# Performance work log

Hardware: AMD Instinct MI355X
Metric: run time of the kernel (lower is better)

## Reference

```python
import jax, jax.numpy as jnp
import numpy as np

N = 100000
E = 1600000
IN_C = 128
HID = 256
OUT_C = 128
MLP_H = 512  # hidden_state_factor * hidden_channels


def _mk_mlp(key, d_in, d_h, d_out):
    ks = jax.random.split(key, 3)
    s = 0.02
    return (
        jax.random.normal(ks[0], (d_in, d_h), jnp.float32) * s, jnp.zeros((d_h,), jnp.float32),
        jax.random.normal(ks[1], (d_h, d_h), jnp.float32) * s, jnp.zeros((d_h,), jnp.float32),
        jax.random.normal(ks[2], (d_h, d_out), jnp.float32) * s, jnp.zeros((d_out,), jnp.float32),
    )


def _mlp(x, w1, b1, w2, b2, w3, b3, last_act):
    h = jax.nn.relu(x @ w1 + b1)
    h = jax.nn.relu(h @ w2 + b2)
    h = h @ w3 + b3
    return jax.nn.relu(h) if last_act else h


def setup_inputs() -> dict:
    key = jax.random.key(0)
    kx, ke, k1, k2, k3 = jax.random.split(key, 5)
    x = jax.random.normal(kx, (N, IN_C), jnp.float32)
    edge_index = jax.random.randint(ke, (2, E), 0, N, jnp.int64)
    enc = _mk_mlp(k1, IN_C, MLP_H, HID)
    conv = _mk_mlp(k2, HID, MLP_H, HID)
    dec = _mk_mlp(k3, HID, MLP_H, OUT_C)
    names_enc = ["enc_w1", "enc_b1", "enc_w2", "enc_b2", "enc_w3", "enc_b3"]
    names_conv = ["conv_w1", "conv_b1", "conv_w2", "conv_b2", "conv_w3", "conv_b3"]
    names_dec = ["dec_w1", "dec_b1", "dec_w2", "dec_b2", "dec_w3", "dec_b3"]
    d = {"x": x, "edge_index": edge_index, "iterations": 1}
    d.update(dict(zip(names_enc, enc)))
    d.update(dict(zip(names_conv, conv)))
    d.update(dict(zip(names_dec, dec)))
    return d


def reference(x, edge_index,
              enc_w1, enc_b1, enc_w2, enc_b2, enc_w3, enc_b3,
              conv_w1, conv_b1, conv_w2, conv_b2, conv_w3, conv_b3,
              dec_w1, dec_b1, dec_w2, dec_b2, dec_w3, dec_b3,
              iterations):
    # encoder MLP (Identity norm, ReLU, dropout=0)
    h = _mlp(x, enc_w1, enc_b1, enc_w2, enc_b2, enc_w3, enc_b3, True)  # [N, HID]
    # GINConv: scatter-add neighbor features (eps=0): agg[i] = sum_{j->i} h[j]
    src, dst = edge_index[0], edge_index[1]
    agg = jax.ops.segment_sum(h[src], dst, num_segments=h.shape[0])  # [N, HID]
    # residual: x = x + conv_mlp(h + agg)
    h = h + _mlp(h + agg, conv_w1, conv_b1, conv_w2, conv_b2, conv_w3, conv_b3, True)
    # decoder MLP without last activation
    return _mlp(h, dec_w1, dec_b1, dec_w2, dec_b2, dec_w3, dec_b3, False)
```

## Files before the change

### kernel.cpp

```cpp
#include <hip/hip_runtime.h>
#include <cstdint>
#include <cstddef>


typedef __attribute__((ext_vector_type(8))) __bf16 bf16x8;
typedef __attribute__((ext_vector_type(4))) float f32x4;

__device__ __forceinline__ unsigned short f2bf(float f) {
    unsigned int u = __float_as_uint(f);
    u += 0x7FFF + ((u >> 16) & 1);
    return (unsigned short)(u >> 16);
}
__device__ __forceinline__ float bf2f(unsigned int s) {
    return __uint_as_float(s << 16);
}

#define FENCE asm volatile("" ::: "memory")

template<bool RELU, bool HAS_RES, bool SF32, bool ORDER>
__global__ __launch_bounds__(256, 2)
void gemm128(const unsigned short* __restrict__ A,
             const unsigned short* __restrict__ Wt,
             const float* __restrict__ Bias,
             const unsigned short* __restrict__ Res,
             float* __restrict__ Cf, unsigned short* __restrict__ Cb,
             int M, int K, int N, int MT, int orderBlocks,
             const int* __restrict__ ei, int* __restrict__ cur,
             int* __restrict__ ssrc, int E)
{
    __shared__ unsigned short As[2][128 * 32];
    __shared__ unsigned short Bs[2][128 * 32];

    const int tid  = threadIdx.x;

    if (ORDER && (int)blockIdx.x < orderBlocks) {
        const int nth = orderBlocks * 256;
        for (int e = (int)blockIdx.x * 256 + tid; e < E; e += nth) {
            const int s = ei[e];
            const int d = ei[E + e];
            const int pos = atomicAdd(&cur[d], 1);
            ssrc[pos] = s;
        }
        return;
    }

    const int bid = ORDER ? ((int)blockIdx.x - orderBlocks) : (int)blockIdx.x;
    const int NT = N >> 7;
    const int total = MT * NT;
    const int q = total >> 3, r = total & 7;
    const int xcd = bid & 7, idx = bid >> 3;
    const int wg = (xcd < r ? xcd * (q + 1) : r * (q + 1) + (xcd - r) * q) + idx;
    const int mtile = wg / NT;
    const int ntile = wg - mtile * NT;
    const int m0 = mtile * 128;
    const int n0 = ntile * 128;

    const int wave = tid >> 6;
    const int lane = tid & 63;
    const int wm = wave >> 1;
    const int wn = wave & 1;

    f32x4 acc[4][4];
#pragma unroll
    for (int i = 0; i < 4; ++i)
#pragma unroll
        for (int j = 0; j < 4; ++j) acc[i][j] = (f32x4){0.f, 0.f, 0.f, 0.f};

    const int srow = lane >> 2;
    const int scol = (((lane & 3) ^ ((lane >> 3) & 3)) << 3);

    auto stage = [&](int buf, int k0) {
#pragma unroll
        for (int i = 0; i < 2; ++i) {
            const int row = (wave << 5) + (i << 4) + srow;
            int gm = m0 + row; gm = (gm < M) ? gm : (M - 1);
            const unsigned short* gp = A + (size_t)gm * K + k0 + scol;
            __builtin_amdgcn_global_load_lds(
                (const __attribute__((address_space(1))) void*)gp,
                (__attribute__((address_space(3))) void*)&As[buf][((wave << 5) + (i << 4)) * 32],
                16, 0, 0);
        }
#pragma unroll
        for (int i = 0; i < 2; ++i) {
            const int row = (wave << 5) + (i << 4) + srow;
            const unsigned short* gp = Wt + (size_t)(n0 + row) * K + k0 + scol;
            __builtin_amdgcn_global_load_lds(
                (const __attribute__((address_space(1))) void*)gp,
                (__attribute__((address_space(3))) void*)&Bs[buf][((wave << 5) + (i << 4)) * 32],
                16, 0, 0);
        }
    };

    const int KT = K >> 5;
    const int lr  = lane & 15;
    const int lkw = lane >> 4;
    const int sw  = (lr >> 1) & 3;

    stage(0, 0);

    int buf = 0;
    for (int t = 0; t < KT; ++t) {
        if (t + 1 < KT) {
            stage(buf ^ 1, (t + 1) << 5);
            asm volatile("s_waitcnt vmcnt(4)" ::: "memory");
        } else {
            asm volatile("s_waitcnt vmcnt(0)" ::: "memory");
        }
        FENCE; __builtin_amdgcn_s_barrier(); FENCE;

        const int ks = (lkw ^ sw) << 3;
        bf16x8 af[4], bg[4];
#pragma unroll
        for (int f = 0; f < 4; ++f) {
            const int ra = wm * 64 + f * 16 + lr;
            af[f] = *(const bf16x8*)&As[buf][ra * 32 + ks];
            const int rb = wn * 64 + f * 16 + lr;
            bg[f] = *(const bf16x8*)&Bs[buf][rb * 32 + ks];
        }
#pragma unroll
        for (int mf = 0; mf < 4; ++mf)
#pragma unroll
            for (int nf = 0; nf < 4; ++nf)
                acc[mf][nf] = __builtin_amdgcn_mfma_f32_16x16x32_bf16(
                    af[mf], bg[nf], acc[mf][nf], 0, 0, 0);

        FENCE; __builtin_amdgcn_s_barrier(); FENCE;
        buf ^= 1;
    }

    const int lg = lane >> 4;
#pragma unroll
    for (int mf = 0; mf < 4; ++mf) {
#pragma unroll
        for (int r2 = 0; r2 < 4; ++r2) {
            const int row = m0 + wm * 64 + mf * 16 + lg * 4 + r2;
            if (row >= M) continue;
#pragma unroll
            for (int nf = 0; nf < 4; ++nf) {
                const int col = n0 + wn * 64 + nf * 16 + lr;
                float v = acc[mf][nf][r2] + Bias[col];
                if (RELU) v = fmaxf(v, 0.f);
                if (HAS_RES) v += bf2f(Res[(size_t)row * N + col]);
                if (SF32) Cf[(size_t)row * N + col] = v;
                else      Cb[(size_t)row * N + col] = f2bf(v);
            }
        }
    }
}

struct PrepArgs {
    const float* W[9];
    unsigned short* Wt[9];
    int wstart[10];
    int Kd[9], Nd[9];
    const float* x;
    unsigned short* xbf;
    const int* ei;
    int* cnt;
    int histBlocks, wtTotal, nCvt4, E;
};

__global__ __launch_bounds__(256)
void prep_kernel(PrepArgs a)
{
    __shared__ unsigned short t[64][72];
    int b = blockIdx.x;
    const int tid = threadIdx.x;
    if (b < a.histBlocks) {
        const int nth = a.histBlocks * 256;
        for (int e = b * 256 + tid; e < a.E; e += nth)
            atomicAdd(&a.cnt[a.ei[a.E + e]], 1);
        return;
    }
    b -= a.histBlocks;
    if (b < a.wtTotal) {
        int job = 0;
        while (b >= a.wstart[job + 1]) ++job;
        const int lb = b - a.wstart[job];
        const int K = a.Kd[job], N = a.Nd[job];
        const int kt = K >> 6;
        const int kb = (lb % kt) * 64, nb = (lb / kt) * 64;
        const float* W = a.W[job];
        unsigned short* Wt = a.Wt[job];
        const int kl = tid >> 4, n4 = (tid & 15) << 2;
#pragma unroll
        for (int it = 0; it < 4; ++it) {
            const int k = kl + it * 16;
            const float4 v = *(const float4*)&W[(size_t)(kb + k) * N + nb + n4];
            t[n4 + 0][k] = f2bf(v.x); t[n4 + 1][k] = f2bf(v.y);
            t[n4 + 2][k] = f2bf(v.z); t[n4 + 3][k] = f2bf(v.w);
        }
        __syncthreads();
        const int n = tid >> 2, kc = (tid & 3) << 4;
        *(uint4*)&Wt[(size_t)(nb + n) * K + kb + kc]     = *(const uint4*)&t[n][kc];
        *(uint4*)&Wt[(size_t)(nb + n) * K + kb + kc + 8] = *(const uint4*)&t[n][kc + 8];
        return;
    }
    b -= a.wtTotal;
    const int i = b * 256 + tid;
    if (i < a.nCvt4) {
        const float4 v = ((const float4*)a.x)[i];
        ushort4 o;
        o.x = f2bf(v.x); o.y = f2bf(v.y); o.z = f2bf(v.z); o.w = f2bf(v.w);
        ((ushort4*)a.xbf)[i] = o;
    }
}

__global__ __launch_bounds__(256)
void zero_ints(int* __restrict__ p, int n)
{
    const int i = blockIdx.x * 256 + threadIdx.x;
    if (i < n) p[i] = 0;
}

__global__ __launch_bounds__(256)
void scan_reduce(const int* __restrict__ cnt, int* __restrict__ bsum, int N)
{
    __shared__ int s[256];
    const int i = blockIdx.x * 256 + threadIdx.x;
    s[threadIdx.x] = (i < N) ? cnt[i] : 0;
    __syncthreads();
#pragma unroll
    for (int off = 128; off > 0; off >>= 1) {
        if (threadIdx.x < off) s[threadIdx.x] += s[threadIdx.x + off];
        __syncthreads();
    }
    if (threadIdx.x == 0) bsum[blockIdx.x] = s[0];
}

__global__ __launch_bounds__(512)
void scan_blocksums(int* __restrict__ bsum, int NB)
{
    __shared__ int a[512], b[512];
    const int t = threadIdx.x;
    const int v = (t < NB) ? bsum[t] : 0;
    a[t] = v;
    __syncthreads();
    int* s = a; int* d = b;
    for (int off = 1; off < 512; off <<= 1) {
        int x = s[t];
        if (t >= off) x += s[t - off];
        d[t] = x;
        __syncthreads();
        int* tmp = s; s = d; d = tmp;
    }
    if (t < NB) bsum[t] = s[t] - v;
}

__global__ __launch_bounds__(256)
void scan_final(const int* __restrict__ cnt, const int* __restrict__ bpre,
                int* __restrict__ off, int* __restrict__ cur, int N)
{
    __shared__ int a[256], b[256];
    const int i = blockIdx.x * 256 + threadIdx.x;
    const int t = threadIdx.x;
    const int v = (i < N) ? cnt[i] : 0;
    a[t] = v;
    __syncthreads();
    int* s = a; int* d = b;
    for (int o = 1; o < 256; o <<= 1) {
        int x = s[t];
        if (t >= o) x += s[t - o];
        d[t] = x;
        __syncthreads();
        int* tmp = s; s = d; d = tmp;
    }
    const int excl = s[t] - v + bpre[blockIdx.x];
    if (i < N) {
        off[i] = excl;
        cur[i] = excl;
        if (i == N - 1) off[N] = excl + v;
    }
}

__global__ __launch_bounds__(256)
void agg_kernel(const unsigned short* __restrict__ hbf, const int* __restrict__ off,
                const int* __restrict__ ssrc, unsigned short* __restrict__ hpg, int Nn)
{
    const int gw   = (int)((blockIdx.x * 256 + threadIdx.x) >> 6);
    const int lane = threadIdx.x & 63;
    const int node = gw >> 1;
    if (node >= Nn) return;
    const int ci = (gw & 1) * 64 + lane;
    const int e0 = off[node], e1 = off[node + 1];
    const unsigned int* base = (const unsigned int*)hbf;

    unsigned int u = base[(size_t)node * 128 + ci];
    float a0 = bf2f(u & 0xffffu), a1 = bf2f(u >> 16);

    int e = e0;
    for (; e + 7 < e1; e += 8) {
        int s[8];
#pragma unroll
        for (int j = 0; j < 8; ++j) s[j] = ssrc[e + j];
        unsigned int v[8];
#pragma unroll
        for (int j = 0; j < 8; ++j) v[j] = base[(size_t)s[j] * 128 + ci];
#pragma unroll
        for (int j = 0; j < 8; ++j) {
            a0 += bf2f(v[j] & 0xffffu);
            a1 += bf2f(v[j] >> 16);
        }
    }
    for (; e + 1 < e1; e += 2) {
        const unsigned int v0 = base[(size_t)ssrc[e]     * 128 + ci];
        const unsigned int v1 = base[(size_t)ssrc[e + 1] * 128 + ci];
        a0 += bf2f(v0 & 0xffffu) + bf2f(v1 & 0xffffu);
        a1 += bf2f(v0 >> 16)     + bf2f(v1 >> 16);
    }
    if (e < e1) {
        const unsigned int v0 = base[(size_t)ssrc[e] * 128 + ci];
        a0 += bf2f(v0 & 0xffffu); a1 += bf2f(v0 >> 16);
    }
    ((unsigned int*)hpg)[(size_t)node * 128 + ci] =
        (unsigned)f2bf(a0) | ((unsigned)f2bf(a1) << 16);
}


extern "C" void kernel_launch(void* const* d_in, const int* in_sizes, int n_in,
                              void* d_out, int out_size, void* d_ws, size_t ws_size,
                              hipStream_t stream)
{
    const float* x  = (const float*)d_in[0];
    const int*   ei = (const int*)d_in[1];
    const float* W[9]  = {(const float*)d_in[3],  (const float*)d_in[5],  (const float*)d_in[7],
                          (const float*)d_in[9],  (const float*)d_in[11], (const float*)d_in[13],
                          (const float*)d_in[15], (const float*)d_in[17], (const float*)d_in[19]};
    const float* B[9]  = {(const float*)d_in[4],  (const float*)d_in[6],  (const float*)d_in[8],
                          (const float*)d_in[10], (const float*)d_in[12], (const float*)d_in[14],
                          (const float*)d_in[16], (const float*)d_in[18], (const float*)d_in[20]};
    const int    Kd[9] = {128, 512, 512, 256, 512, 512, 256, 512, 512};
    const int    Nd[9] = {512, 512, 256, 512, 512, 256, 512, 512, 128};
    float* out = (float*)d_out;

    const int M = 100000;
    const int E = 1600000;
    const size_t HN = (size_t)M * 256;
    const int ORDER_BLOCKS = 768;
    const int HIST_BLOCKS  = 1024;

    char* p = (char*)d_ws;
    auto carve = [&](size_t bytes) -> char* {
        char* r = p;
        p += (bytes + 255) & ~(size_t)255;
        return r;
    };
    unsigned short* hbf   = (unsigned short*)carve(HN * 2);
    unsigned short* hpgbf = (unsigned short*)carve(HN * 2);
    unsigned short* xbf   = (unsigned short*)carve((size_t)M * 128 * 2);
    unsigned short* Wt[9];
    for (int i = 0; i < 9; ++i) Wt[i] = (unsigned short*)carve((size_t)Kd[i] * Nd[i] * 2);
    int* cnt  = (int*)carve(M * 4);
    int* off  = (int*)carve((M + 4) * 4);
    int* cur  = (int*)carve(M * 4);
    int* bsum = (int*)carve(512 * 4);
    int* ssrc = (int*)carve((size_t)E * 4);

    const size_t fixed = (size_t)(p - (char*)d_ws);
    size_t remain = (ws_size > fixed) ? ws_size - fixed : 0;
    size_t cap = remain / (2 * 512 * 2);
    if (cap < 4096) cap = 4096;
    const int nch = (cap >= (size_t)M) ? 1 : (int)((M + cap - 1) / cap);
    const int CH = (M + nch - 1) / nch;
    unsigned short* t1 = (unsigned short*)carve((size_t)CH * 512 * 2);
    unsigned short* t2 = (unsigned short*)carve((size_t)CH * 512 * 2);

    const dim3 blk(256);
    const int NB = (M + 255) / 256;

    zero_ints<<<NB, blk, 0, stream>>>(cnt, M);

    PrepArgs pa;
    pa.wstart[0] = 0;
    for (int i = 0; i < 9; ++i) {
        pa.W[i] = W[i]; pa.Wt[i] = Wt[i]; pa.Kd[i] = Kd[i]; pa.Nd[i] = Nd[i];
        pa.wstart[i + 1] = pa.wstart[i] + (Kd[i] / 64) * (Nd[i] / 64);
    }
    pa.x = x; pa.xbf = xbf; pa.ei = ei; pa.cnt = cnt;
    pa.histBlocks = HIST_BLOCKS;
    pa.wtTotal = pa.wstart[9];
    pa.nCvt4 = M * 128 / 4;
    pa.E = E;
    const int cvtBlocks = (pa.nCvt4 + 255) / 256;
    prep_kernel<<<HIST_BLOCKS + pa.wtTotal + cvtBlocks, blk, 0, stream>>>(pa);

    scan_reduce<<<NB, blk, 0, stream>>>(cnt, bsum, M);
    scan_blocksums<<<1, 512, 0, stream>>>(bsum, NB);
    scan_final<<<NB, blk, 0, stream>>>(cnt, bsum, off, cur, M);

    auto mt = [](int m) { return (m + 127) / 128; };

    for (int m0 = 0; m0 < M; m0 += CH) {
        const int cm = (M - m0 < CH) ? (M - m0) : CH;
        const int MT = mt(cm);
        gemm128<true, false, false, false><<<MT * 4, blk, 0, stream>>>(
            xbf + (size_t)m0 * 128, Wt[0], B[0], nullptr, nullptr, t1,
            cm, 128, 512, MT, 0, nullptr, nullptr, nullptr, 0);
        if (m0 == 0) {
            gemm128<true, false, false, true><<<ORDER_BLOCKS + MT * 4, blk, 0, stream>>>(
                t1, Wt[1], B[1], nullptr, nullptr, t2, cm, 512, 512, MT,
                ORDER_BLOCKS, ei, cur, ssrc, E);
        } else {
            gemm128<true, false, false, false><<<MT * 4, blk, 0, stream>>>(
                t1, Wt[1], B[1], nullptr, nullptr, t2, cm, 512, 512, MT,
                0, nullptr, nullptr, nullptr, 0);
        }
        gemm128<true, false, false, false><<<MT * 2, blk, 0, stream>>>(
            t2, Wt[2], B[2], nullptr, nullptr, hbf + (size_t)m0 * 256, cm, 512, 256, MT,
            0, nullptr, nullptr, nullptr, 0);
    }

    agg_kernel<<<(int)(((size_t)2 * M * 64 + 255) / 256), blk, 0, stream>>>(
        hbf, off, ssrc, hpgbf, M);

    for (int m0 = 0; m0 < M; m0 += CH) {
        const int cm = (M - m0 < CH) ? (M - m0) : CH;
        const int MT = mt(cm);
        gemm128<true, false, false, false><<<MT * 4, blk, 0, stream>>>(
            hpgbf + (size_t)m0 * 256, Wt[3], B[3], nullptr, nullptr, t1, cm, 256, 512, MT,
            0, nullptr, nullptr, nullptr, 0);
        gemm128<true, false, false, false><<<MT * 4, blk, 0, stream>>>(
            t1, Wt[4], B[4], nullptr, nullptr, t2, cm, 512, 512, MT,
            0, nullptr, nullptr, nullptr, 0);
        gemm128<true, true, false, false><<<MT * 2, blk, 0, stream>>>(
            t2, Wt[5], B[5], hbf + (size_t)m0 * 256, nullptr, hpgbf + (size_t)m0 * 256,
            cm, 512, 256, MT, 0, nullptr, nullptr, nullptr, 0);
    }

    for (int m0 = 0; m0 < M; m0 += CH) {
        const int cm = (M - m0 < CH) ? (M - m0) : CH;
        const int MT = mt(cm);
        gemm128<true, false, false, false><<<MT * 4, blk, 0, stream>>>(
            hpgbf + (size_t)m0 * 256, Wt[6], B[6], nullptr, nullptr, t1, cm, 256, 512, MT,
            0, nullptr, nullptr, nullptr, 0);
        gemm128<true, false, false, false><<<MT * 4, blk, 0, stream>>>(
            t1, Wt[7], B[7], nullptr, nullptr, t2, cm, 512, 512, MT,
            0, nullptr, nullptr, nullptr, 0);
        gemm128<false, false, true, false><<<MT, blk, 0, stream>>>(
            t2, Wt[8], B[8], nullptr, out + (size_t)m0 * 128, nullptr, cm, 512, 128, MT,
            0, nullptr, nullptr, nullptr, 0);
    }
}
```

Before: 866.4 us.

## Split edge ordering across first three GEMMs and batch aggregation index loads

The edge-ordering (CSR fill via atomics) work is now split into three edge ranges, each piggybacked on one of the first-chunk encoder GEMM launches, so the atomic scatter overlaps more GEMM work. Fewer ordering blocks are used per launch. The aggregation kernel now loads 16 source indices cooperatively with one load per lane and broadcasts them with readlane, issuing 16 gathers per batch with predicated accumulation. This cuts per-lane redundant index loads but may waste gathers on low-degree nodes, since every batch issues 16 loads regardless of how many edges remain.

```diff
diff --git a/kernel.cpp b/kernel.cpp
--- a/kernel.cpp
+++ b/kernel.cpp
@@ -26,7 +26,7 @@
              float* __restrict__ Cf, unsigned short* __restrict__ Cb,
              int M, int K, int N, int MT, int orderBlocks,
              const int* __restrict__ ei, int* __restrict__ cur,
-             int* __restrict__ ssrc, int E)
+             int* __restrict__ ssrc, int E, int eOff, int eEnd)
 {
     __shared__ unsigned short As[2][128 * 32];
     __shared__ unsigned short Bs[2][128 * 32];
@@ -35,7 +35,7 @@
 
     if (ORDER && (int)blockIdx.x < orderBlocks) {
         const int nth = orderBlocks * 256;
-        for (int e = (int)blockIdx.x * 256 + tid; e < E; e += nth) {
+        for (int e = eOff + (int)blockIdx.x * 256 + tid; e < eEnd; e += nth) {
             const int s = ei[e];
             const int d = ei[E + e];
             const int pos = atomicAdd(&cur[d], 1);
@@ -288,29 +288,28 @@
     unsigned int u = base[(size_t)node * 128 + ci];
     float a0 = bf2f(u & 0xffffu), a1 = bf2f(u >> 16);
 
-    int e = e0;
-    for (; e + 7 < e1; e += 8) {
-        int s[8];
-#pragma unroll
-        for (int j = 0; j < 8; ++j) s[j] = ssrc[e + j];
-        unsigned int v[8];
-#pragma unroll
-        for (int j = 0; j < 8; ++j) v[j] = base[(size_t)s[j] * 128 + ci];
-#pragma unroll
-        for (int j = 0; j < 8; ++j) {
-            a0 += bf2f(v[j] & 0xffffu);
-            a1 += bf2f(v[j] >> 16);
-        }
-    }
-    for (; e + 1 < e1; e += 2) {
-        const unsigned int v0 = base[(size_t)ssrc[e]     * 128 + ci];
-        const unsigned int v1 = base[(size_t)ssrc[e + 1] * 128 + ci];
-        a0 += bf2f(v0 & 0xffffu) + bf2f(v1 & 0xffffu);
-        a1 += bf2f(v0 >> 16)     + bf2f(v1 >> 16);
-    }
-    if (e < e1) {
-        const unsigned int v0 = base[(size_t)ssrc[e] * 128 + ci];
-        a0 += bf2f(v0 & 0xffffu); a1 += bf2f(v0 >> 16);
+    for (int b = e0; b < e1; b += 16) {
+        const int idx = b + (lane & 15);
+        const int sv  = (idx < e1) ? ssrc[idx] : 0;
+        const int cnt = e1 - b;
+
+        int sj[16];
+#pragma unroll
+        for (int j = 0; j < 16; ++j)
+            sj[j] = __builtin_amdgcn_readlane(sv, j);
+
+        unsigned int v[16];
+#pragma unroll
+        for (int j = 0; j < 16; ++j)
+            v[j] = base[(size_t)sj[j] * 128 + ci];
+
+#pragma unroll
+        for (int j = 0; j < 16; ++j) {
+            if (j < cnt) {
+                a0 += bf2f(v[j] & 0xffffu);
+                a1 += bf2f(v[j] >> 16);
+            }
+        }
     }
     ((unsigned int*)hpg)[(size_t)node * 128 + ci] =
         (unsigned)f2bf(a0) | ((unsigned)f2bf(a1) << 16);
@@ -336,8 +335,10 @@
     const int M = 100000;
     const int E = 1600000;
     const size_t HN = (size_t)M * 256;
-    const int ORDER_BLOCKS = 768;
+    const int ORDER_BLOCKS = 512;
     const int HIST_BLOCKS  = 1024;
+    const int ECUT1 = 533376;
+    const int ECUT2 = 1066752;
 
     char* p = (char*)d_ws;
     auto carve = [&](size_t bytes) -> char* {
@@ -393,21 +394,27 @@
     for (int m0 = 0; m0 < M; m0 += CH) {
         const int cm = (M - m0 < CH) ? (M - m0) : CH;
         const int MT = mt(cm);
-        gemm128<true, false, false, false><<<MT * 4, blk, 0, stream>>>(
-            xbf + (size_t)m0 * 128, Wt[0], B[0], nullptr, nullptr, t1,
-            cm, 128, 512, MT, 0, nullptr, nullptr, nullptr, 0);
         if (m0 == 0) {
             gemm128<true, false, false, true><<<ORDER_BLOCKS + MT * 4, blk, 0, stream>>>(
+                xbf, Wt[0], B[0], nullptr, nullptr, t1, cm, 128, 512, MT,
+                ORDER_BLOCKS, ei, cur, ssrc, E, 0, ECUT1);
+            gemm128<true, false, false, true><<<ORDER_BLOCKS + MT * 4, blk, 0, stream>>>(
                 t1, Wt[1], B[1], nullptr, nullptr, t2, cm, 512, 512, MT,
-                ORDER_BLOCKS, ei, cur, ssrc, E);
+                ORDER_BLOCKS, ei, cur, ssrc, E, ECUT1, ECUT2);
+            gemm128<true, false, false, true><<<ORDER_BLOCKS + MT * 2, blk, 0, stream>>>(
+                t2, Wt[2], B[2], nullptr, nullptr, hbf, cm, 512, 256, MT,
+                ORDER_BLOCKS, ei, cur, ssrc, E, ECUT2, E);
         } else {
             gemm128<true, false, false, false><<<MT * 4, blk, 0, stream>>>(
+                xbf + (size_t)m0 * 128, Wt[0], B[0], nullptr, nullptr, t1,
+                cm, 128, 512, MT, 0, nullptr, nullptr, nullptr, 0, 0, 0);
+            gemm128<true, false, false, false><<<MT * 4, blk, 0, stream>>>(
                 t1, Wt[1], B[1], nullptr, nullptr, t2, cm, 512, 512, MT,
-                0, nullptr, nullptr, nullptr, 0);
-        }
-        gemm128<true, false, false, false><<<MT * 2, blk, 0, stream>>>(
-            t2, Wt[2], B[2], nullptr, nullptr, hbf + (size_t)m0 * 256, cm, 512, 256, MT,
-            0, nullptr, nullptr, nullptr, 0);
+                0, nullptr, nullptr, nullptr, 0, 0, 0);
+            gemm128<true, false, false, false><<<MT * 2, blk, 0, stream>>>(
+                t2, Wt[2], B[2], nullptr, nullptr, hbf + (size_t)m0 * 256, cm, 512, 256, MT,
+                0, nullptr, nullptr, nullptr, 0, 0, 0);
+        }
     }
 
     agg_kernel<<<(int)(((size_t)2 * M * 64 + 255) / 256), blk, 0, stream>>>(
@@ -418,13 +425,13 @@
         const int MT = mt(cm);
         gemm128<true, false, false, false><<<MT * 4, blk, 0, stream>>>(
             hpgbf + (size_t)m0 * 256, Wt[3], B[3], nullptr, nullptr, t1, cm, 256, 512, MT,
-            0, nullptr, nullptr, nullptr, 0);
+            0, nullptr, nullptr, nullptr, 0, 0, 0);
         gemm128<true, false, false, false><<<MT * 4, blk, 0, stream>>>(
             t1, Wt[4], B[4], nullptr, nullptr, t2, cm, 512, 512, MT,
-            0, nullptr, nullptr, nullptr, 0);
+            0, nullptr, nullptr, nullptr, 0, 0, 0);
         gemm128<true, true, false, false><<<MT * 2, blk, 0, stream>>>(
             t2, Wt[5], B[5], hbf + (size_t)m0 * 256, nullptr, hpgbf + (size_t)m0 * 256,
-            cm, 512, 256, MT, 0, nullptr, nullptr, nullptr, 0);
+            cm, 512, 256, MT, 0, nullptr, nullptr, nullptr, 0, 0, 0);
     }
 
     for (int m0 = 0; m0 < M; m0 += CH) {
@@ -432,12 +439,12 @@
         const int MT = mt(cm);
         gemm128<true, false, false, false><<<MT * 4, blk, 0, stream>>>(
             hpgbf + (size_t)m0 * 256, Wt[6], B[6], nullptr, nullptr, t1, cm, 256, 512, MT,
-            0, nullptr, nullptr, nullptr, 0);
+            0, nullptr, nullptr, nullptr, 0, 0, 0);
         gemm128<true, false, false, false><<<MT * 4, blk, 0, stream>>>(
             t1, Wt[7], B[7], nullptr, nullptr, t2, cm, 512, 512, MT,
-            0, nullptr, nullptr, nullptr, 0);
+            0, nullptr, nullptr, nullptr, 0, 0, 0);
         gemm128<false, false, true, false><<<MT, blk, 0, stream>>>(
             t2, Wt[8], B[8], nullptr, out + (size_t)m0 * 128, nullptr, cm, 512, 128, MT,
-            0, nullptr, nullptr, nullptr, 0);
-    }
-}
+            0, nullptr, nullptr, nullptr, 0, 0, 0);
+    }
+}
```

After: 837.5 us. -3.3%, faster.
